# Kernel tuning notes

Hardware: AMD Instinct MI355X
Metric: run time of the kernel (lower is better)

The kernel has to match this reference:

```python
import jax, jax.numpy as jnp
import numpy as np
from jax import lax

N = 4194304
DELTA_T = 1.0
ETA = 1.0
QN = 1.5 * 3600.0
INITIAL_X2 = 1.0


def setup_inputs() -> dict:
    key = jax.random.key(0)
    k1, k2, k3 = jax.random.split(key, 3)
    return {
        "uk_sequence": jax.random.normal(k1, (N,), dtype=jnp.float32),
        "Rp": jnp.float32(1.0),
        "Cp": jnp.float32(1.0),
        "R0": jax.random.uniform(k2, (), dtype=jnp.float32),
        "a_coeffs": jax.random.normal(k3, (9,), dtype=jnp.float32) * 0.1,
    }


def _forward(uk_sequence, Rp, Cp, R0, a_coeffs):
    # Diagonal linear SSM, state = (x1, x2)
    A00 = jnp.exp(-DELTA_T / (Rp * Cp))            # decay of RC branch
    B0 = Rp * (1.0 - A00)                           # input gain on x1
    B1 = jnp.float32(-ETA * DELTA_T / QN)           # constant coulomb-counting gain

    def step(carry, u):
        x1, x2 = carry
        nxt = (A00 * x1 + B0 * u, x2 + B1 * u)
        return nxt, carry                           # emit state BEFORE update (xk[k])

    init = (jnp.float32(0.0), jnp.float32(INITIAL_X2))
    _, (x1s, x2s) = lax.scan(step, init, uk_sequence)  # each [N]

    # poly8(x2) = a0 + a1*x2 + ... + a8*x2^8 via Horner (highest-first for polyval)
    poly = jnp.polyval(a_coeffs[::-1], x2s)
    y = poly - x1s - R0 * uk_sequence               # [N]
    return y[:, None]                               # [N, 1] to match torch output


def reference(uk_sequence, Rp, Cp, R0, a_coeffs):
    return _forward(uk_sequence, Rp, Cp, R0, a_coeffs)
```

## Files before the change

### kernel.cpp

```cpp
#include <hip/hip_runtime.h>


constexpr int    BLOCK = 256;
constexpr int    TPER  = 16;
constexpr int    CHUNK = BLOCK * TPER;
constexpr int    NTOT  = 4194304;
constexpr int    NB    = NTOT / CHUNK;

__global__ __launch_bounds__(BLOCK) void k1_agg(
    const float* __restrict__ u,
    const float* __restrict__ Rp_p, const float* __restrict__ Cp_p,
    double* __restrict__ wsS, double* __restrict__ wsP)
{
    __shared__ double sS[BLOCK];
    __shared__ double sPm[BLOCK];
    const int b = blockIdx.x, t = threadIdx.x;
    const double invRC = 1.0 / ((double)Rp_p[0] * (double)Cp_p[0]);
    const double A00 = exp(-invRC);

    const float4* up = (const float4*)(u + (size_t)b * CHUNK + (size_t)t * TPER);
    float4 v[4];
    v[0] = up[0]; v[1] = up[1]; v[2] = up[2]; v[3] = up[3];
    const float* uu = (const float*)v;

    double s = 0.0, p = 0.0;
#pragma unroll
    for (int i = 0; i < TPER; ++i) { s = A00 * s + (double)uu[i]; p += (double)uu[i]; }
    sS[t] = s; sPm[t] = p;
    __syncthreads();

    double f = exp(-(double)TPER * invRC);
    for (int stride = 1; stride < BLOCK; stride <<= 1) {
        if ((t & (2 * stride - 1)) == 0) {
            sS[t]  = sS[t] * f + sS[t + stride];
            sPm[t] = sPm[t] + sPm[t + stride];
        }
        f *= f;
        __syncthreads();
    }
    if (t == 0) { wsS[b] = sS[0]; wsP[b] = sPm[0]; }
}

__global__ __launch_bounds__(NB) void k2_scan(
    const float* __restrict__ Rp_p, const float* __restrict__ Cp_p,
    const double* __restrict__ wsS, const double* __restrict__ wsP,
    double* __restrict__ wsWc, double* __restrict__ wsPc)
{
    __shared__ double sW[2][NB];
    __shared__ double sP[2][NB];
    const int t = threadIdx.x;
    const double invRC = 1.0 / ((double)Rp_p[0] * (double)Cp_p[0]);

    sW[0][t] = wsS[t]; sP[0][t] = wsP[t];
    __syncthreads();

    double f = exp(-(double)CHUNK * invRC);
    int cur = 0;
    for (int d = 1; d < NB; d <<= 1) {
        const int nxt = cur ^ 1;
        double w = sW[cur][t], p = sP[cur][t];
        if (t >= d) { w = sW[cur][t - d] * f + w; p = sP[cur][t - d] + p; }
        sW[nxt][t] = w; sP[nxt][t] = p;
        cur = nxt; f *= f;
        __syncthreads();
    }
    wsWc[t] = (t == 0) ? 0.0 : sW[cur][t - 1];
    wsPc[t] = (t == 0) ? 0.0 : sP[cur][t - 1];
}

__global__ __launch_bounds__(BLOCK) void k3_emit(
    const float* __restrict__ u,
    const float* __restrict__ Rp_p, const float* __restrict__ Cp_p,
    const float* __restrict__ R0_p, const float* __restrict__ ac,
    const double* __restrict__ wsWc, const double* __restrict__ wsPc,
    float* __restrict__ out)
{
    __shared__ double sS[2][BLOCK];
    __shared__ double sP[2][BLOCK];
    const int b = blockIdx.x, t = threadIdx.x;
    const double Rp = (double)Rp_p[0], Cp = (double)Cp_p[0];
    const double invRC = 1.0 / (Rp * Cp);
    const double A00 = exp(-invRC);
    const double B0  = Rp * (1.0 - A00);
    const double B1  = -1.0 / 5400.0;
    const double R0  = (double)R0_p[0];
    double a[9];
#pragma unroll
    for (int i = 0; i < 9; ++i) a[i] = (double)ac[i];

    const size_t base = (size_t)b * CHUNK + (size_t)t * TPER;
    const float4* up = (const float4*)(u + base);
    float4 v[4];
    v[0] = up[0]; v[1] = up[1]; v[2] = up[2]; v[3] = up[3];
    const float* uu = (const float*)v;

    double s = 0.0, p = 0.0;
#pragma unroll
    for (int i = 0; i < TPER; ++i) { s = A00 * s + (double)uu[i]; p += (double)uu[i]; }
    sS[0][t] = s; sP[0][t] = p;
    __syncthreads();

    double f = exp(-(double)TPER * invRC);
    int cur = 0;
    for (int d = 1; d < BLOCK; d <<= 1) {
        const int nxt = cur ^ 1;
        double w = sS[cur][t], q = sP[cur][t];
        if (t >= d) { w = sS[cur][t - d] * f + w; q = sP[cur][t - d] + q; }
        sS[nxt][t] = w; sP[nxt][t] = q;
        cur = nxt; f *= f;
        __syncthreads();
    }
    const double exW = (t == 0) ? 0.0 : sS[cur][t - 1];
    const double exP = (t == 0) ? 0.0 : sP[cur][t - 1];
    const double W0 = wsWc[b], P0 = wsPc[b];

    double Wcur = exp(-(double)(TPER * t) * invRC) * W0 + exW;
    double Pcur = P0 + exP;

    float4 o[4];
    float* oy = (float*)o;
#pragma unroll
    for (int i = 0; i < TPER; ++i) {
        const double x2 = 1.0 + B1 * Pcur;
        const double x1 = B0 * Wcur;
        double poly = a[8];
#pragma unroll
        for (int j = 7; j >= 0; --j) poly = poly * x2 + a[j];
        oy[i] = (float)(poly - x1 - R0 * (double)uu[i]);
        Wcur = A00 * Wcur + (double)uu[i];
        Pcur += (double)uu[i];
    }
    float4* op = (float4*)(out + base);
    op[0] = o[0]; op[1] = o[1]; op[2] = o[2]; op[3] = o[3];
}

extern "C" void kernel_launch(void* const* d_in, const int* in_sizes, int n_in,
                              void* d_out, int out_size, void* d_ws, size_t ws_size,
                              hipStream_t stream) {
    const float* u    = (const float*)d_in[0];
    const float* Rp_p = (const float*)d_in[1];
    const float* Cp_p = (const float*)d_in[2];
    const float* R0_p = (const float*)d_in[3];
    const float* ac   = (const float*)d_in[4];
    float* out = (float*)d_out;

    double* ws   = (double*)d_ws;
    double* wsS  = ws;
    double* wsP  = ws + NB;
    double* wsWc = ws + 2 * NB;
    double* wsPc = ws + 3 * NB;

    k1_agg <<<NB, BLOCK, 0, stream>>>(u, Rp_p, Cp_p, wsS, wsP);
    k2_scan<<<1,  NB,    0, stream>>>(Rp_p, Cp_p, wsS, wsP, wsWc, wsPc);
    k3_emit<<<NB, BLOCK, 0, stream>>>(u, Rp_p, Cp_p, R0_p, ac, wsWc, wsPc, out);
}
```

Baseline: 89.11 us.

## Fuse three-pass scan into single-pass decoupled look-back kernel

```diff
diff --git a/kernel.cpp b/kernel.cpp
--- a/kernel.cpp
+++ b/kernel.cpp
@@ -1,94 +1,63 @@
 #include <hip/hip_runtime.h>
+#include <cstddef>
 
 
-constexpr int    BLOCK = 256;
-constexpr int    TPER  = 16;
-constexpr int    CHUNK = BLOCK * TPER;
-constexpr int    NTOT  = 4194304;
-constexpr int    NB    = NTOT / CHUNK;
+constexpr int BLOCK = 256;
+constexpr int TPER  = 16;
+constexpr int CHUNK = BLOCK * TPER;
+constexpr int NTOT  = 4194304;
+constexpr int NB    = NTOT / CHUNK;
 
-__global__ __launch_bounds__(BLOCK) void k1_agg(
-    const float* __restrict__ u,
-    const float* __restrict__ Rp_p, const float* __restrict__ Cp_p,
-    double* __restrict__ wsS, double* __restrict__ wsP)
-{
-    __shared__ double sS[BLOCK];
-    __shared__ double sPm[BLOCK];
-    const int b = blockIdx.x, t = threadIdx.x;
-    const double invRC = 1.0 / ((double)Rp_p[0] * (double)Cp_p[0]);
-    const double A00 = exp(-invRC);
+struct ScanWS {
+    int    flags[NB];
+    int    ticket;
+    int    _pad[15];
+    double aggP[NB];
+    double aggW[NB];
+    double inclP[NB];
+    double inclW[NB];
+};
 
-    const float4* up = (const float4*)(u + (size_t)b * CHUNK + (size_t)t * TPER);
-    float4 v[4];
-    v[0] = up[0]; v[1] = up[1]; v[2] = up[2]; v[3] = up[3];
-    const float* uu = (const float*)v;
-
-    double s = 0.0, p = 0.0;
-#pragma unroll
-    for (int i = 0; i < TPER; ++i) { s = A00 * s + (double)uu[i]; p += (double)uu[i]; }
-    sS[t] = s; sPm[t] = p;
-    __syncthreads();
-
-    double f = exp(-(double)TPER * invRC);
-    for (int stride = 1; stride < BLOCK; stride <<= 1) {
-        if ((t & (2 * stride - 1)) == 0) {
-            sS[t]  = sS[t] * f + sS[t + stride];
-            sPm[t] = sPm[t] + sPm[t + stride];
-        }
-        f *= f;
-        __syncthreads();
-    }
-    if (t == 0) { wsS[b] = sS[0]; wsP[b] = sPm[0]; }
+__device__ inline void store_d(double* p, double v) {
+    __hip_atomic_store((unsigned long long*)p,
+                       __builtin_bit_cast(unsigned long long, v),
+                       __ATOMIC_RELAXED, __HIP_MEMORY_SCOPE_AGENT);
+}
+__device__ inline double load_d(const double* p) {
+    unsigned long long x = __hip_atomic_load((const unsigned long long*)p,
+                                             __ATOMIC_RELAXED, __HIP_MEMORY_SCOPE_AGENT);
+    return __builtin_bit_cast(double, x);
 }
 
-__global__ __launch_bounds__(NB) void k2_scan(
-    const float* __restrict__ Rp_p, const float* __restrict__ Cp_p,
-    const double* __restrict__ wsS, const double* __restrict__ wsP,
-    double* __restrict__ wsWc, double* __restrict__ wsPc)
-{
-    __shared__ double sW[2][NB];
-    __shared__ double sP[2][NB];
-    const int t = threadIdx.x;
-    const double invRC = 1.0 / ((double)Rp_p[0] * (double)Cp_p[0]);
-
-    sW[0][t] = wsS[t]; sP[0][t] = wsP[t];
-    __syncthreads();
-
-    double f = exp(-(double)CHUNK * invRC);
-    int cur = 0;
-    for (int d = 1; d < NB; d <<= 1) {
-        const int nxt = cur ^ 1;
-        double w = sW[cur][t], p = sP[cur][t];
-        if (t >= d) { w = sW[cur][t - d] * f + w; p = sP[cur][t - d] + p; }
-        sW[nxt][t] = w; sP[nxt][t] = p;
-        cur = nxt; f *= f;
-        __syncthreads();
-    }
-    wsWc[t] = (t == 0) ? 0.0 : sW[cur][t - 1];
-    wsPc[t] = (t == 0) ? 0.0 : sP[cur][t - 1];
-}
-
-__global__ __launch_bounds__(BLOCK) void k3_emit(
+__global__ __launch_bounds__(BLOCK) void fused_scan(
     const float* __restrict__ u,
     const float* __restrict__ Rp_p, const float* __restrict__ Cp_p,
     const float* __restrict__ R0_p, const float* __restrict__ ac,
-    const double* __restrict__ wsWc, const double* __restrict__ wsPc,
+    ScanWS* __restrict__ ws,
     float* __restrict__ out)
 {
     __shared__ double sS[2][BLOCK];
     __shared__ double sP[2][BLOCK];
-    const int b = blockIdx.x, t = threadIdx.x;
-    const double Rp = (double)Rp_p[0], Cp = (double)Cp_p[0];
+    __shared__ int    s_bid;
+    __shared__ double s_cP, s_cW;
+
+    const int t = threadIdx.x;
+    if (t == 0)
+        s_bid = __hip_atomic_fetch_add(&ws->ticket, 1, __ATOMIC_RELAXED,
+                                       __HIP_MEMORY_SCOPE_AGENT);
+
+    const double Rp    = (double)Rp_p[0], Cp = (double)Cp_p[0];
     const double invRC = 1.0 / (Rp * Cp);
-    const double A00 = exp(-invRC);
-    const double B0  = Rp * (1.0 - A00);
-    const double B1  = -1.0 / 5400.0;
-    const double R0  = (double)R0_p[0];
-    double a[9];
-#pragma unroll
-    for (int i = 0; i < 9; ++i) a[i] = (double)ac[i];
+    const double A00   = exp(-invRC);
+    const double B0    = Rp * (1.0 - A00);
+    const double B1    = -1.0 / 5400.0;
+    const double R0    = (double)R0_p[0];
+    const double dC    = exp(-(double)CHUNK * invRC);
 
-    const size_t base = (size_t)b * CHUNK + (size_t)t * TPER;
+    __syncthreads();
+    const int bid = s_bid;
+
+    const size_t base = (size_t)bid * CHUNK + (size_t)t * TPER;
     const float4* up = (const float4*)(u + base);
     float4 v[4];
     v[0] = up[0]; v[1] = up[1]; v[2] = up[2]; v[3] = up[3];
@@ -110,23 +79,100 @@
         cur = nxt; f *= f;
         __syncthreads();
     }
-    const double exW = (t == 0) ? 0.0 : sS[cur][t - 1];
-    const double exP = (t == 0) ? 0.0 : sP[cur][t - 1];
-    const double W0 = wsWc[b], P0 = wsPc[b];
+    const double exW  = t ? sS[cur][t - 1] : 0.0;
+    const double exP  = t ? sP[cur][t - 1] : 0.0;
+    const double totW = sS[cur][BLOCK - 1];
+    const double totP = sP[cur][BLOCK - 1];
 
-    double Wcur = exp(-(double)(TPER * t) * invRC) * W0 + exW;
-    double Pcur = P0 + exP;
+    if (t == 0) {
+        if (bid == 0) {
+            store_d(&ws->inclP[0], totP);
+            store_d(&ws->inclW[0], totW);
+            __hip_atomic_store(&ws->flags[0], 2, __ATOMIC_RELEASE,
+                               __HIP_MEMORY_SCOPE_AGENT);
+            s_cP = 0.0; s_cW = 0.0;
+        } else {
+            store_d(&ws->aggP[bid], totP);
+            store_d(&ws->aggW[bid], totW);
+            __hip_atomic_store(&ws->flags[bid], 1, __ATOMIC_RELEASE,
+                               __HIP_MEMORY_SCOPE_AGENT);
+        }
+    }
+
+    if (bid > 0 && t < 64) {
+        double carry = 0.0;
+        int end = bid;
+        for (;;) {
+            const int idx = end - 64 + t;
+            int fl = 0;
+            if (idx >= 0) {
+                fl = __hip_atomic_load(&ws->flags[idx], __ATOMIC_ACQUIRE,
+                                       __HIP_MEMORY_SCOPE_AGENT);
+                while (fl == 0) {
+                    __builtin_amdgcn_s_sleep(1);
+                    fl = __hip_atomic_load(&ws->flags[idx], __ATOMIC_ACQUIRE,
+                                           __HIP_MEMORY_SCOPE_AGENT);
+                }
+            }
+            const unsigned long long incl = __ballot(fl == 2);
+            const int hl = incl ? (63 - __builtin_clzll(incl)) : 0;
+            double val = 0.0;
+            if (idx >= 0 && (!incl || t >= hl))
+                val = (incl && t == hl) ? load_d(&ws->inclP[idx])
+                                        : load_d(&ws->aggP[idx]);
+            for (int off = 32; off; off >>= 1) val += __shfl_down(val, off, 64);
+            carry += val;
+            if (incl) break;
+            end -= 64;
+            if (end <= 0) break;
+        }
+        if (t == 0) {
+            double cW;
+            if (dC == 0.0) {
+                int fl1 = __hip_atomic_load(&ws->flags[bid - 1], __ATOMIC_ACQUIRE,
+                                            __HIP_MEMORY_SCOPE_AGENT);
+                while (fl1 == 0) {
+                    __builtin_amdgcn_s_sleep(1);
+                    fl1 = __hip_atomic_load(&ws->flags[bid - 1], __ATOMIC_ACQUIRE,
+                                            __HIP_MEMORY_SCOPE_AGENT);
+                }
+                cW = (fl1 == 2) ? load_d(&ws->inclW[bid - 1])
+                                : load_d(&ws->aggW[bid - 1]);
+            } else {
+                int fl1;
+                do {
+                    fl1 = __hip_atomic_load(&ws->flags[bid - 1], __ATOMIC_ACQUIRE,
+                                            __HIP_MEMORY_SCOPE_AGENT);
+                    if (fl1 != 2) __builtin_amdgcn_s_sleep(1);
+                } while (fl1 != 2);
+                cW = load_d(&ws->inclW[bid - 1]);
+            }
+            s_cP = carry; s_cW = cW;
+            store_d(&ws->inclP[bid], carry + totP);
+            store_d(&ws->inclW[bid], cW * dC + totW);
+            __hip_atomic_store(&ws->flags[bid], 2, __ATOMIC_RELEASE,
+                               __HIP_MEMORY_SCOPE_AGENT);
+        }
+    }
+    __syncthreads();
+    const double cP = s_cP, cWb = s_cW;
+
+    double a[9];
+#pragma unroll
+    for (int i = 0; i < 9; ++i) a[i] = (double)ac[i];
+
+    double Wcur = cWb * exp(-(double)(TPER * t) * invRC) + exW;
+    double Pcur = cP + exP;
 
     float4 o[4];
     float* oy = (float*)o;
 #pragma unroll
     for (int i = 0; i < TPER; ++i) {
         const double x2 = 1.0 + B1 * Pcur;
-        const double x1 = B0 * Wcur;
         double poly = a[8];
 #pragma unroll
         for (int j = 7; j >= 0; --j) poly = poly * x2 + a[j];
-        oy[i] = (float)(poly - x1 - R0 * (double)uu[i]);
+        oy[i] = (float)(poly - B0 * Wcur - R0 * (double)uu[i]);
         Wcur = A00 * Wcur + (double)uu[i];
         Pcur += (double)uu[i];
     }
@@ -143,14 +189,8 @@
     const float* R0_p = (const float*)d_in[3];
     const float* ac   = (const float*)d_in[4];
     float* out = (float*)d_out;
+    ScanWS* ws = (ScanWS*)d_ws;
 
-    double* ws   = (double*)d_ws;
-    double* wsS  = ws;
-    double* wsP  = ws + NB;
-    double* wsWc = ws + 2 * NB;
-    double* wsPc = ws + 3 * NB;
-
-    k1_agg <<<NB, BLOCK, 0, stream>>>(u, Rp_p, Cp_p, wsS, wsP);
-    k2_scan<<<1,  NB,    0, stream>>>(Rp_p, Cp_p, wsS, wsP, wsWc, wsPc);
-    k3_emit<<<NB, BLOCK, 0, stream>>>(u, Rp_p, Cp_p, R0_p, ac, wsWc, wsPc, out);
+    hipMemsetAsync(d_ws, 0, offsetof(ScanWS, aggP), stream);
+    fused_scan<<<NB, BLOCK, 0, stream>>>(u, Rp_p, Cp_p, R0_p, ac, ws, out);
 }
```

New measurement: 192.7 us. 116% more time.

## Fuse carry scan into emit kernel via per-block decoupled prefix reduction

Applied to the files above, without the earlier changes.

```diff
diff --git a/kernel.cpp b/kernel.cpp
--- a/kernel.cpp
+++ b/kernel.cpp
@@ -1,104 +1,104 @@
 #include <hip/hip_runtime.h>
 
 
-constexpr int    BLOCK = 256;
-constexpr int    TPER  = 16;
-constexpr int    CHUNK = BLOCK * TPER;
-constexpr int    NTOT  = 4194304;
-constexpr int    NB    = NTOT / CHUNK;
+constexpr int BLOCK = 256;
+constexpr int TPER  = 8;
+constexpr int CHUNK = BLOCK * TPER;
+constexpr int NTOT  = 4194304;
+constexpr int NB    = NTOT / CHUNK;
+constexpr int APT   = NB / BLOCK;
 
-__global__ __launch_bounds__(BLOCK) void k1_agg(
+__global__ __launch_bounds__(BLOCK) void kA_agg(
     const float* __restrict__ u,
     const float* __restrict__ Rp_p, const float* __restrict__ Cp_p,
-    double* __restrict__ wsS, double* __restrict__ wsP)
+    double* __restrict__ aggW, double* __restrict__ aggP)
 {
-    __shared__ double sS[BLOCK];
-    __shared__ double sPm[BLOCK];
+    __shared__ double sW[BLOCK];
+    __shared__ double sP[BLOCK];
     const int b = blockIdx.x, t = threadIdx.x;
     const double invRC = 1.0 / ((double)Rp_p[0] * (double)Cp_p[0]);
-    const double A00 = exp(-invRC);
+    const double A00   = exp(-invRC);
 
     const float4* up = (const float4*)(u + (size_t)b * CHUNK + (size_t)t * TPER);
-    float4 v[4];
-    v[0] = up[0]; v[1] = up[1]; v[2] = up[2]; v[3] = up[3];
+    float4 v[2];
+    v[0] = up[0]; v[1] = up[1];
     const float* uu = (const float*)v;
 
     double s = 0.0, p = 0.0;
 #pragma unroll
     for (int i = 0; i < TPER; ++i) { s = A00 * s + (double)uu[i]; p += (double)uu[i]; }
-    sS[t] = s; sPm[t] = p;
+    sW[t] = s; sP[t] = p;
     __syncthreads();
 
     double f = exp(-(double)TPER * invRC);
     for (int stride = 1; stride < BLOCK; stride <<= 1) {
         if ((t & (2 * stride - 1)) == 0) {
-            sS[t]  = sS[t] * f + sS[t + stride];
-            sPm[t] = sPm[t] + sPm[t + stride];
+            sW[t] = sW[t] * f + sW[t + stride];
+            sP[t] = sP[t] + sP[t + stride];
         }
         f *= f;
         __syncthreads();
     }
-    if (t == 0) { wsS[b] = sS[0]; wsP[b] = sPm[0]; }
+    if (t == 0) { aggW[b] = sW[0]; aggP[b] = sP[0]; }
 }
 
-__global__ __launch_bounds__(NB) void k2_scan(
-    const float* __restrict__ Rp_p, const float* __restrict__ Cp_p,
-    const double* __restrict__ wsS, const double* __restrict__ wsP,
-    double* __restrict__ wsWc, double* __restrict__ wsPc)
-{
-    __shared__ double sW[2][NB];
-    __shared__ double sP[2][NB];
-    const int t = threadIdx.x;
-    const double invRC = 1.0 / ((double)Rp_p[0] * (double)Cp_p[0]);
-
-    sW[0][t] = wsS[t]; sP[0][t] = wsP[t];
-    __syncthreads();
-
-    double f = exp(-(double)CHUNK * invRC);
-    int cur = 0;
-    for (int d = 1; d < NB; d <<= 1) {
-        const int nxt = cur ^ 1;
-        double w = sW[cur][t], p = sP[cur][t];
-        if (t >= d) { w = sW[cur][t - d] * f + w; p = sP[cur][t - d] + p; }
-        sW[nxt][t] = w; sP[nxt][t] = p;
-        cur = nxt; f *= f;
-        __syncthreads();
-    }
-    wsWc[t] = (t == 0) ? 0.0 : sW[cur][t - 1];
-    wsPc[t] = (t == 0) ? 0.0 : sP[cur][t - 1];
-}
-
-__global__ __launch_bounds__(BLOCK) void k3_emit(
+__global__ __launch_bounds__(BLOCK) void kB_emit(
     const float* __restrict__ u,
     const float* __restrict__ Rp_p, const float* __restrict__ Cp_p,
     const float* __restrict__ R0_p, const float* __restrict__ ac,
-    const double* __restrict__ wsWc, const double* __restrict__ wsPc,
+    const double* __restrict__ aggW, const double* __restrict__ aggP,
     float* __restrict__ out)
 {
     __shared__ double sS[2][BLOCK];
     __shared__ double sP[2][BLOCK];
+    __shared__ double sRed[BLOCK / 64];
+    __shared__ double sCW;
+
     const int b = blockIdx.x, t = threadIdx.x;
-    const double Rp = (double)Rp_p[0], Cp = (double)Cp_p[0];
+    const double Rp    = (double)Rp_p[0], Cp = (double)Cp_p[0];
     const double invRC = 1.0 / (Rp * Cp);
-    const double A00 = exp(-invRC);
-    const double B0  = Rp * (1.0 - A00);
-    const double B1  = -1.0 / 5400.0;
-    const double R0  = (double)R0_p[0];
-    double a[9];
-#pragma unroll
-    for (int i = 0; i < 9; ++i) a[i] = (double)ac[i];
+    const double A00   = exp(-invRC);
+    const double B0    = Rp * (1.0 - A00);
+    const double B1    = -1.0 / 5400.0;
+    const double R0    = (double)R0_p[0];
+    const double dC    = exp(-(double)CHUNK * invRC);
 
     const size_t base = (size_t)b * CHUNK + (size_t)t * TPER;
     const float4* up = (const float4*)(u + base);
-    float4 v[4];
-    v[0] = up[0]; v[1] = up[1]; v[2] = up[2]; v[3] = up[3];
+    float4 v[2];
+    v[0] = up[0]; v[1] = up[1];
     const float* uu = (const float*)v;
+
+    double pc = 0.0;
+#pragma unroll
+    for (int i = 0; i < APT; ++i) {
+        const int j = t * APT + i;
+        if (j < b) pc += aggP[j];
+    }
+    for (int off = 32; off; off >>= 1) pc += __shfl_down(pc, off, 64);
+    if ((t & 63) == 0) sRed[t >> 6] = pc;
+
+    if (t == 0) {
+        double cW;
+        if (dC == 0.0) {
+            cW = (b > 0) ? aggW[b - 1] : 0.0;
+        } else {
+            cW = 0.0;
+            for (int j = 0; j < b; ++j) cW = cW * dC + aggW[j];
+        }
+        sCW = cW;
+    }
 
     double s = 0.0, p = 0.0;
 #pragma unroll
     for (int i = 0; i < TPER; ++i) { s = A00 * s + (double)uu[i]; p += (double)uu[i]; }
     sS[0][t] = s; sP[0][t] = p;
     __syncthreads();
+
+    double carryP = 0.0;
+#pragma unroll
+    for (int w = 0; w < BLOCK / 64; ++w) carryP += sRed[w];
+    const double carryW = sCW;
 
     double f = exp(-(double)TPER * invRC);
     int cur = 0;
@@ -110,28 +110,30 @@
         cur = nxt; f *= f;
         __syncthreads();
     }
-    const double exW = (t == 0) ? 0.0 : sS[cur][t - 1];
-    const double exP = (t == 0) ? 0.0 : sP[cur][t - 1];
-    const double W0 = wsWc[b], P0 = wsPc[b];
+    const double exW = t ? sS[cur][t - 1] : 0.0;
+    const double exP = t ? sP[cur][t - 1] : 0.0;
 
-    double Wcur = exp(-(double)(TPER * t) * invRC) * W0 + exW;
-    double Pcur = P0 + exP;
+    double a[9];
+#pragma unroll
+    for (int i = 0; i < 9; ++i) a[i] = (double)ac[i];
 
-    float4 o[4];
+    double Wcur = carryW * exp(-(double)(TPER * t) * invRC) + exW;
+    double Pcur = carryP + exP;
+
+    float4 o[2];
     float* oy = (float*)o;
 #pragma unroll
     for (int i = 0; i < TPER; ++i) {
         const double x2 = 1.0 + B1 * Pcur;
-        const double x1 = B0 * Wcur;
         double poly = a[8];
 #pragma unroll
         for (int j = 7; j >= 0; --j) poly = poly * x2 + a[j];
-        oy[i] = (float)(poly - x1 - R0 * (double)uu[i]);
+        oy[i] = (float)(poly - B0 * Wcur - R0 * (double)uu[i]);
         Wcur = A00 * Wcur + (double)uu[i];
         Pcur += (double)uu[i];
     }
     float4* op = (float4*)(out + base);
-    op[0] = o[0]; op[1] = o[1]; op[2] = o[2]; op[3] = o[3];
+    op[0] = o[0]; op[1] = o[1];
 }
 
 extern "C" void kernel_launch(void* const* d_in, const int* in_sizes, int n_in,
@@ -144,13 +146,9 @@
     const float* ac   = (const float*)d_in[4];
     float* out = (float*)d_out;
 
-    double* ws   = (double*)d_ws;
-    double* wsS  = ws;
-    double* wsP  = ws + NB;
-    double* wsWc = ws + 2 * NB;
-    double* wsPc = ws + 3 * NB;
+    double* wsW = (double*)d_ws;
+    double* wsP = (double*)d_ws + NB;
 
-    k1_agg <<<NB, BLOCK, 0, stream>>>(u, Rp_p, Cp_p, wsS, wsP);
-    k2_scan<<<1,  NB,    0, stream>>>(Rp_p, Cp_p, wsS, wsP, wsWc, wsPc);
-    k3_emit<<<NB, BLOCK, 0, stream>>>(u, Rp_p, Cp_p, R0_p, ac, wsWc, wsPc, out);
+    kA_agg <<<NB, BLOCK, 0, stream>>>(u, Rp_p, Cp_p, wsW, wsP);
+    kB_emit<<<NB, BLOCK, 0, stream>>>(u, Rp_p, Cp_p, R0_p, ac, wsW, wsP, out);
 }
```

Measured after the change: 87.50 us. No clear change (-1.8%).
